# Kernel tuning notes

Measured on AMD Instinct MI355X. Metric: run time of the kernel, lower is better.

## Reference

```python
import jax, jax.numpy as jnp
import numpy as np

RADIUS = 0.2
NSAMPLE = 32
EPS = 1e-5  # BatchNorm2d default eps


def _bn_relu(x, g, b):
    # BatchNorm2d in training mode: per-channel stats over (B, S, nsample), biased var.
    m = x.mean(axis=(0, 1, 2))
    v = jnp.mean((x - m) ** 2, axis=(0, 1, 2))
    return jax.nn.relu((x - m) * jax.lax.rsqrt(v + EPS) * g + b)


def setup_inputs() -> dict:
    key = jax.random.key(0)
    ks = jax.random.split(key, 8)
    B, N, S = 8, 8192, 2048
    xyz = jax.random.uniform(ks[0], (B, 3, N), dtype=jnp.float32)          # unit cube
    points = jax.random.normal(ks[1], (B, 3, N), dtype=jnp.float32)
    fps_idx = jax.random.randint(ks[2], (B, S), 0, N, dtype=jnp.int32)
    W1 = jax.random.normal(ks[3], (64, 6), dtype=jnp.float32) * 0.1
    W2 = jax.random.normal(ks[4], (64, 64), dtype=jnp.float32) * 0.1
    W3 = jax.random.normal(ks[5], (128, 64), dtype=jnp.float32) * 0.1
    return dict(
        xyz=xyz, points=points, fps_idx=fps_idx,
        W1=W1, g1=jnp.ones((64,)), b1=jnp.zeros((64,)),
        W2=W2, g2=jnp.ones((64,)), b2=jnp.zeros((64,)),
        W3=W3, g3=jnp.ones((128,)), b3=jnp.zeros((128,)),
    )


def reference(xyz, points, fps_idx, W1, g1, b1, W2, g2, b2, W3, g3, b3):
    B, _, N = xyz.shape
    xyz_t = jnp.transpose(xyz, (0, 2, 1))            # [B,N,3]
    pts_t = jnp.transpose(points, (0, 2, 1))         # [B,N,D]
    # gather_operation: sampled centers
    new_xyz_t = jnp.take_along_axis(xyz_t, fps_idx[:, :, None], axis=1)  # [B,S,3]
    # ball query: first NSAMPLE points within radius; pad with first hit
    d2 = jnp.sum((new_xyz_t[:, :, None, :] - xyz_t[:, None, :, :]) ** 2, axis=-1)  # [B,S,N]
    keys = jnp.where(d2 <= RADIUS * RADIUS, jnp.arange(N, dtype=jnp.int32), N)
    neg_top, _ = jax.lax.top_k(-keys, NSAMPLE)       # smallest keys first
    idx = -neg_top                                   # [B,S,NSAMPLE]
    idx = jnp.where(idx < N, idx, idx[:, :, 0:1])    # pad empty slots with first hit (self always in-radius)
    bidx = jnp.arange(B)[:, None, None]
    grouped_xyz = xyz_t[bidx, idx]                   # [B,S,ns,3]
    rel = grouped_xyz - new_xyz_t[:, :, None, :]     # center-relative coords
    grouped_pts = pts_t[bidx, idx]                   # [B,S,ns,D]
    feat = jnp.concatenate([rel, grouped_pts], axis=-1)  # [B,S,ns,3+D]
    for W, g, b in ((W1, g1, b1), (W2, g2, b2), (W3, g3, b3)):
        feat = _bn_relu(jnp.einsum('bsnc,oc->bsno', feat, W), g, b)
    new_points = jnp.max(feat, axis=2)               # max over neighbors -> [B,S,C]
    return jnp.transpose(new_xyz_t, (0, 2, 1)), jnp.transpose(new_points, (0, 2, 1))
```

## Files before the change

kernel.cpp:

```cpp
#include <hip/hip_runtime.h>
#include <hip/hip_bf16.h>

#define BB_ 8
#define NN_ 8192
#define SS_ 2048
#define NS 32
#define C1 64
#define C2 64
#define C3 128
#define RAD2 0.04f
#define BN_EPS 1e-5f
#define M_TOT (BB_*SS_*NS)
#define INV_M (1.0f/524288.0f)
#define YSTR 34

typedef __attribute__((ext_vector_type(8))) short bf16x8;
typedef __attribute__((ext_vector_type(4))) float f32x4;

#define FBF_OFF 0
#define WPK_OFF 2097152
#define ST_OFF  2104320
#define GMM_OFF 2104832

__device__ inline unsigned pkbf(float a, float b) {
    __hip_bfloat162 h = __float22bfloat162_rn(make_float2(a, b));
    unsigned r; __builtin_memcpy(&r, &h, 4); return r;
}
__device__ inline bf16x8 asfrag(uint4 v) { bf16x8 r; __builtin_memcpy(&r, &v, 16); return r; }
__device__ inline float bflo(unsigned u) { unsigned x = u << 16; float f; __builtin_memcpy(&f, &x, 4); return f; }
__device__ inline float bfhi(unsigned u) { unsigned x = u & 0xffff0000u; float f; __builtin_memcpy(&f, &x, 4); return f; }

__device__ inline void fin1_ch(const float* __restrict__ st, const float* __restrict__ W1,
                               const float* __restrict__ g, const float* __restrict__ bb,
                               int o, float* __restrict__ al, float* __restrict__ cl) {
    float w[6];
    #pragma unroll
    for (int i = 0; i < 6; ++i) w[i] = W1[o * 6 + i];
    float ms = 0.f;
    #pragma unroll
    for (int i = 0; i < 6; ++i) ms = fmaf(w[i], st[i], ms);
    float m = ms * INV_M;
    float e2 = 0.f;
    #pragma unroll
    for (int ci = 0; ci < 6; ++ci)
        #pragma unroll
        for (int d = 0; d < 6; ++d) {
            int lo = ci < d ? ci : d, hi = ci < d ? d : ci;
            int idx = 6 + lo * 6 - lo * (lo + 1) / 2 + hi;
            e2 = fmaf(w[ci] * w[d], st[idx], e2);
        }
    float var = e2 * INV_M - m * m;
    float ai = g[o] * (1.0f / sqrtf(var + BN_EPS));
    al[o] = ai;
    cl[o] = bb[o] - m * ai;
}

__device__ inline void fin_ch(const float* __restrict__ sum, const float* __restrict__ sq,
                              const float* __restrict__ g, const float* __restrict__ bb,
                              int o, float* __restrict__ al, float* __restrict__ cl) {
    float m = sum[o] * INV_M;
    float var = sq[o] * INV_M - m * m;
    float ai = g[o] * (1.0f / sqrtf(var + BN_EPS));
    al[o] = ai;
    cl[o] = bb[o] - m * ai;
}

__global__ void k_front(const float* __restrict__ xyz, const float* __restrict__ pts,
                        const int* __restrict__ fps, uint4* __restrict__ fbf,
                        const float* __restrict__ W1, const float* __restrict__ W2,
                        const float* __restrict__ W3, uint4* __restrict__ wf,
                        float* __restrict__ st) {
    __shared__ int lidx[4][NS];
    int tid = threadIdx.x;
    if (blockIdx.x >= 4096) {
        int bb = blockIdx.x - 4096;
        if (bb == 7) { st[tid] = 0.f; st[tid + 256] = 0.f; return; }
        int t = bb * 256 + tid;
        int l = t & 63, p = l & 15, qd = l >> 4;
        float v[8];
        if (t < 256) {
            int mt = t >> 6;
            #pragma unroll
            for (int j = 0; j < 8; ++j)
                v[j] = (qd == 0 && j < 6) ? W1[(mt * 16 + p) * 6 + j] : 0.f;
        } else if (t < 768) {
            int fr = (t - 256) >> 6;
            int mt = fr >> 1, kf = fr & 1;
            #pragma unroll
            for (int j = 0; j < 8; ++j)
                v[j] = W2[(16 * mt + p) * 64 + kf * 32 + qd * 8 + j];
        } else {
            int fr = (t - 768) >> 6;
            int nt = fr >> 1, kf = fr & 1;
            #pragma unroll
            for (int j = 0; j < 8; ++j)
                v[j] = W3[(nt * 16 + p) * 64 + kf * 32 + qd * 8 + j];
        }
        uint4 o;
        o.x = pkbf(v[0], v[1]); o.y = pkbf(v[2], v[3]);
        o.z = pkbf(v[4], v[5]); o.w = pkbf(v[6], v[7]);
        wf[t] = o;
        return;
    }
    int wave = (blockIdx.x * blockDim.x + tid) >> 6;
    int lane = tid & 63;
    int wslot = tid >> 6;
    int b = wave / SS_;
    const float* xb = xyz + (size_t)b * 3 * NN_;
    const float* pb = pts + (size_t)b * 3 * NN_;
    int ci = fps[wave];
    float cx = xb[ci], cy = xb[NN_ + ci], cz = xb[2 * NN_ + ci];

    float sx[4], sy[4], sz[4];
    #pragma unroll
    for (int k = 0; k < 4; ++k) {
        sx[k] = xb[k * 64 + lane];
        sy[k] = xb[NN_ + k * 64 + lane];
        sz[k] = xb[2 * NN_ + k * 64 + lane];
    }
    int found = 0;
    int first_i = -1;
    #pragma unroll 1
    for (int base = 0; base < NN_; base += 256) {
        #pragma unroll
        for (int k = 0; k < 4; ++k) {
            float xv = sx[k], yv = sy[k], zv = sz[k];
            int nb = base + 256 + k * 64;
            if (nb >= NN_) nb = 0;
            sx[k] = xb[nb + lane];
            sy[k] = xb[NN_ + nb + lane];
            sz[k] = xb[2 * NN_ + nb + lane];
            float dx = xv - cx, dy = yv - cy, dz = zv - cz;
            float d2 = __fadd_rn(__fadd_rn(__fmul_rn(dx, dx), __fmul_rn(dy, dy)), __fmul_rn(dz, dz));
            bool inr = d2 <= RAD2;
            unsigned long long mask = __ballot(inr);
            if (first_i < 0 && mask) first_i = base + k * 64 + __builtin_ctzll(mask);
            if (inr) {
                int pos = found + __popcll(mask & ((1ull << lane) - 1ull));
                if (pos < NS) lidx[wslot][pos] = base + k * 64 + lane;
            }
            found += __popcll(mask);
        }
        if (found >= NS) break;
    }
    if (found > NS) found = NS;
    if (lane < NS) {
        int j = (lane < found) ? lidx[wslot][lane] : first_i;
        uint4 o;
        o.x = pkbf(xb[j] - cx,           xb[NN_ + j] - cy);
        o.y = pkbf(xb[2 * NN_ + j] - cz, pb[j]);
        o.z = pkbf(pb[NN_ + j],          pb[2 * NN_ + j]);
        o.w = 0u;
        fbf[(size_t)wave * NS + lane] = o;
    }
}

__global__ void k_p1(const uint4* __restrict__ fbf, float* __restrict__ st) {
    __shared__ float sacc[27];
    int tid = threadIdx.x;
    if (tid < 27) sacc[tid] = 0.f;
    __syncthreads();
    int gt = blockIdx.x * 256 + tid;
    float vals[27];
    #pragma unroll
    for (int i = 0; i < 27; ++i) vals[i] = 0.f;
    #pragma unroll 1
    for (int it = 0; it < M_TOT / 262144; ++it) {
        uint4 w = fbf[it * 262144 + gt];
        float f[6] = { bflo(w.x), bfhi(w.x), bflo(w.y), bfhi(w.y), bflo(w.z), bfhi(w.z) };
        #pragma unroll
        for (int c = 0; c < 6; ++c) vals[c] += f[c];
        int q = 6;
        #pragma unroll
        for (int c = 0; c < 6; ++c)
            #pragma unroll
            for (int d = c; d < 6; ++d) { vals[q] = fmaf(f[c], f[d], vals[q]); ++q; }
    }
    int lane = tid & 63;
    #pragma unroll
    for (int i = 0; i < 27; ++i) {
        float v = vals[i];
        #pragma unroll
        for (int d = 32; d; d >>= 1) v += __shfl_xor(v, d);
        if (lane == 0) atomicAdd(&sacc[i], v);
    }
    __syncthreads();
    if (tid < 27) atomicAdd(&st[tid], sacc[tid]);
}

__global__ __launch_bounds__(256, 4) void k_p2(
        const uint4* __restrict__ fbf, const uint4* __restrict__ wpk,
        float* __restrict__ st,
        const float* __restrict__ W1, const float* __restrict__ g1, const float* __restrict__ b1) {
    __shared__ unsigned yls[4][64 * YSTR];
    __shared__ float bs[C2], bq[C2];
    __shared__ float a1ls[C1], c1ls[C1];
    int tid = threadIdx.x, wslot = tid >> 6, lane = tid & 63;
    int p = lane & 15, qd = lane >> 4;
    int tile0 = blockIdx.x * 8 + wslot;
    uint4 bv[4];
    #pragma unroll
    for (int nt = 0; nt < 4; ++nt) {
        uint4 v = make_uint4(0u, 0u, 0u, 0u);
        if (qd == 0) v = fbf[tile0 * 64 + nt * 16 + p];
        bv[nt] = v;
    }
    bf16x8 w1r[4];
    #pragma unroll
    for (int mt = 0; mt < 4; ++mt) w1r[mt] = asfrag(wpk[mt * 64 + lane]);
    if (tid < C2) { bs[tid] = 0.f; bq[tid] = 0.f; fin1_ch(st, W1, g1, b1, tid, a1ls, c1ls); }
    __syncthreads();
    const uint4* w2f = wpk + 256;
    unsigned* my = yls[wslot];
    float s2[4][4], q2[4][4];
    #pragma unroll
    for (int i = 0; i < 4; ++i)
        #pragma unroll
        for (int r = 0; r < 4; ++r) { s2[i][r] = 0.f; q2[i][r] = 0.f; }

    #pragma unroll
    for (int t = 0; t < 2; ++t) {
        uint4 nbv[4];
        if (t == 0) {
            #pragma unroll
            for (int nt = 0; nt < 4; ++nt) {
                uint4 v = make_uint4(0u, 0u, 0u, 0u);
                if (qd == 0) v = fbf[(tile0 + 4) * 64 + nt * 16 + p];
                nbv[nt] = v;
            }
        }
        bf16x8 B1[4];
        #pragma unroll
        for (int nt = 0; nt < 4; ++nt) B1[nt] = asfrag(bv[nt]);
        #pragma unroll
        for (int mt = 0; mt < 4; ++mt) {
            bf16x8 A = w1r[mt];
            float4 av = *(const float4*)(a1ls + mt * 16 + qd * 4);
            float4 cv = *(const float4*)(c1ls + mt * 16 + qd * 4);
            #pragma unroll
            for (int nt = 0; nt < 4; ++nt) {
                f32x4 acc = {0.f, 0.f, 0.f, 0.f};
                acc = __builtin_amdgcn_mfma_f32_16x16x32_bf16(A, B1[nt], acc, 0, 0, 0);
                float y0 = fmaxf(fmaf(av.x, acc[0], cv.x), 0.f);
                float y1 = fmaxf(fmaf(av.y, acc[1], cv.y), 0.f);
                float y2 = fmaxf(fmaf(av.z, acc[2], cv.z), 0.f);
                float y3 = fmaxf(fmaf(av.w, acc[3], cv.w), 0.f);
                int a = (nt * 16 + p) * YSTR + mt * 8 + qd * 2;
                *(uint2*)&my[a] = make_uint2(pkbf(y0, y1), pkbf(y2, y3));
            }
        }
        asm volatile("" ::: "memory");
        bf16x8 B2[4][2];
        #pragma unroll
        for (int nt = 0; nt < 4; ++nt)
            #pragma unroll
            for (int kf = 0; kf < 2; ++kf)
                B2[nt][kf] = asfrag(*(const uint4*)&my[(nt * 16 + p) * YSTR + kf * 16 + qd * 4]);
        asm volatile("" ::: "memory");
        #pragma unroll
        for (int mt = 0; mt < 4; ++mt) {
            f32x4 acc[4];
            #pragma unroll
            for (int nt = 0; nt < 4; ++nt) acc[nt] = (f32x4){0.f, 0.f, 0.f, 0.f};
            #pragma unroll
            for (int kf = 0; kf < 2; ++kf) {
                bf16x8 W = asfrag(w2f[(mt * 2 + kf) * 64 + lane]);
                #pragma unroll
                for (int nt = 0; nt < 4; ++nt)
                    acc[nt] = __builtin_amdgcn_mfma_f32_16x16x32_bf16(W, B2[nt][kf], acc[nt], 0, 0, 0);
            }
            #pragma unroll
            for (int r = 0; r < 4; ++r) {
                float u0 = acc[0][r], u1 = acc[1][r], u2 = acc[2][r], u3 = acc[3][r];
                s2[mt][r] += (u0 + u1) + (u2 + u3);
                q2[mt][r] = fmaf(u0, u0, fmaf(u1, u1, fmaf(u2, u2, fmaf(u3, u3, q2[mt][r]))));
            }
        }
        if (t == 0) {
            #pragma unroll
            for (int nt = 0; nt < 4; ++nt) bv[nt] = nbv[nt];
        }
        asm volatile("" ::: "memory");
    }
    #pragma unroll
    for (int mt = 0; mt < 4; ++mt)
        #pragma unroll
        for (int r = 0; r < 4; ++r) {
            float s = s2[mt][r], q = q2[mt][r];
            #pragma unroll
            for (int off = 1; off <= 8; off <<= 1) { s += __shfl_xor(s, off); q += __shfl_xor(q, off); }
            if (p == 0) {
                atomicAdd(&bs[mt * 16 + qd * 4 + r], s);
                atomicAdd(&bq[mt * 16 + qd * 4 + r], q);
            }
        }
    __syncthreads();
    if (tid < C2) { atomicAdd(&st[64 + tid], bs[tid]); atomicAdd(&st[128 + tid], bq[tid]); }
}

__global__ __launch_bounds__(256, 4) void k_p3_fused(
        const uint4* __restrict__ fbf, const uint4* __restrict__ wpk,
        float* __restrict__ st,
        const float* __restrict__ W1, const float* __restrict__ g1, const float* __restrict__ b1,
        const float* __restrict__ g2, const float* __restrict__ b2,
        const float* __restrict__ g3, float* __restrict__ gmm) {
    __shared__ unsigned yls[4][64 * YSTR];
    __shared__ float bs[C3], bq[C3];
    __shared__ float a1ls[C1], c1ls[C1], a2ls[C2], c2ls[C2];
    int tid = threadIdx.x, wslot = tid >> 6, lane = tid & 63;
    int p = lane & 15, qd = lane >> 4;
    int tile0 = blockIdx.x * 4 + wslot;
    uint4 bv0[4], bv1[4];
    #pragma unroll
    for (int nt = 0; nt < 4; ++nt) {
        uint4 v0 = make_uint4(0u, 0u, 0u, 0u);
        uint4 v1 = make_uint4(0u, 0u, 0u, 0u);
        if (qd == 0) {
            v0 = fbf[tile0 * 64 + nt * 16 + p];
            v1 = fbf[(tile0 + 4096) * 64 + nt * 16 + p];
        }
        bv0[nt] = v0; bv1[nt] = v1;
    }
    unsigned posm = 0;
    #pragma unroll
    for (int i = 0; i < 8; ++i) posm |= (g3[i * 16 + p] >= 0.f) ? (1u << i) : 0u;
    if (tid < 128) bs[tid] = 0.f; else bq[tid - 128] = 0.f;
    if (tid < 64) fin1_ch(st, W1, g1, b1, tid, a1ls, c1ls);
    else if (tid < 128) fin_ch(st + 64, st + 128, g2, b2, tid - 64, a2ls, c2ls);
    __syncthreads();
    const uint4* w1f = wpk;
    const uint4* w2f = wpk + 256;
    const uint4* w3f = wpk + 768;
    unsigned* my = yls[wslot];

    #pragma unroll
    for (int it = 0; it < 2; ++it) {
        int tile = tile0 + it * 4096;
        #pragma unroll
        for (int mt = 0; mt < 4; ++mt) {
            bf16x8 Aw = asfrag(w1f[mt * 64 + lane]);
            float4 av = *(const float4*)(a1ls + mt * 16 + qd * 4);
            float4 cv = *(const float4*)(c1ls + mt * 16 + qd * 4);
            #pragma unroll
            for (int nt = 0; nt < 4; ++nt) {
                uint4 bcur = (it == 0) ? bv0[nt] : bv1[nt];
                f32x4 acc = {0.f, 0.f, 0.f, 0.f};
                acc = __builtin_amdgcn_mfma_f32_16x16x32_bf16(Aw, asfrag(bcur), acc, 0, 0, 0);
                float y0 = fmaxf(fmaf(av.x, acc[0], cv.x), 0.f);
                float y1 = fmaxf(fmaf(av.y, acc[1], cv.y), 0.f);
                float y2 = fmaxf(fmaf(av.z, acc[2], cv.z), 0.f);
                float y3 = fmaxf(fmaf(av.w, acc[3], cv.w), 0.f);
                int a = (nt * 16 + p) * YSTR + mt * 8 + qd * 2;
                *(uint2*)&my[a] = make_uint2(pkbf(y0, y1), pkbf(y2, y3));
            }
        }
        asm volatile("" ::: "memory");
        bf16x8 B2[4][2];
        #pragma unroll
        for (int nt = 0; nt < 4; ++nt)
            #pragma unroll
            for (int kf = 0; kf < 2; ++kf)
                B2[nt][kf] = asfrag(*(const uint4*)&my[(nt * 16 + p) * YSTR + kf * 16 + qd * 4]);
        asm volatile("" ::: "memory");
        #pragma unroll
        for (int mt = 0; mt < 4; ++mt) {
            f32x4 acc[4];
            #pragma unroll
            for (int nt = 0; nt < 4; ++nt) acc[nt] = (f32x4){0.f, 0.f, 0.f, 0.f};
            #pragma unroll
            for (int kf = 0; kf < 2; ++kf) {
                bf16x8 W = asfrag(w2f[(mt * 2 + kf) * 64 + lane]);
                #pragma unroll
                for (int nt = 0; nt < 4; ++nt)
                    acc[nt] = __builtin_amdgcn_mfma_f32_16x16x32_bf16(W, B2[nt][kf], acc[nt], 0, 0, 0);
            }
            float4 av = *(const float4*)(a2ls + mt * 16 + qd * 4);
            float4 cv = *(const float4*)(c2ls + mt * 16 + qd * 4);
            #pragma unroll
            for (int nt = 0; nt < 4; ++nt) {
                float y0 = fmaxf(fmaf(av.x, acc[nt][0], cv.x), 0.f);
                float y1 = fmaxf(fmaf(av.y, acc[nt][1], cv.y), 0.f);
                float y2 = fmaxf(fmaf(av.z, acc[nt][2], cv.z), 0.f);
                float y3 = fmaxf(fmaf(av.w, acc[nt][3], cv.w), 0.f);
                int a = (nt * 16 + p) * YSTR + mt * 8 + qd * 2;
                *(uint2*)&my[a] = make_uint2(pkbf(y0, y1), pkbf(y2, y3));
            }
        }
        asm volatile("" ::: "memory");
        bf16x8 A3[4][2];
        #pragma unroll
        for (int mt = 0; mt < 4; ++mt) {
            A3[mt][0] = asfrag(*(const uint4*)&my[(mt * 16 + p) * YSTR + qd * 4]);
            A3[mt][1] = asfrag(*(const uint4*)&my[(mt * 16 + p) * YSTR + 16 + qd * 4]);
        }
        asm volatile("" ::: "memory");
        uint4 wva = w3f[lane];
        uint4 wvb = w3f[64 + lane];
        #pragma unroll 1
        for (int nt = 0; nt < 8; ++nt) {
            int nn = (nt < 7) ? nt + 1 : 7;
            uint4 nwa = w3f[(nn * 2 + 0) * 64 + lane];
            uint4 nwb = w3f[(nn * 2 + 1) * 64 + lane];
            bf16x8 Wa = asfrag(wva), Wb = asfrag(wvb);
            f32x4 acc[4];
            #pragma unroll
            for (int mt = 0; mt < 4; ++mt) {
                acc[mt] = __builtin_amdgcn_mfma_f32_16x16x32_bf16(A3[mt][0], Wa,
                            (f32x4){0.f, 0.f, 0.f, 0.f}, 0, 0, 0);
                acc[mt] = __builtin_amdgcn_mfma_f32_16x16x32_bf16(A3[mt][1], Wb, acc[mt], 0, 0, 0);
            }
            bool pn = (posm >> nt) & 1;
            float s = 0.f, q = 0.f, va = 0.f, vb = 0.f;
            #pragma unroll
            for (int mt = 0; mt < 4; ++mt) {
                float v0 = acc[mt][0], v1 = acc[mt][1], v2 = acc[mt][2], v3 = acc[mt][3];
                s += (v0 + v1) + (v2 + v3);
                q = fmaf(v0, v0, fmaf(v1, v1, fmaf(v2, v2, fmaf(v3, v3, q))));
                float mx = fmaxf(fmaxf(v0, v1), fmaxf(v2, v3));
                float mn = fminf(fminf(v0, v1), fminf(v2, v3));
                float vv = pn ? mx : -mn;
                if (mt == 0) va = vv;
                else if (mt == 1) va = fmaxf(va, vv);
                else if (mt == 2) vb = vv;
                else vb = fmaxf(vb, vv);
            }
            s += __shfl_xor(s, 16); s += __shfl_xor(s, 32);
            q += __shfl_xor(q, 16); q += __shfl_xor(q, 32);
            va = fmaxf(va, __shfl_xor(va, 16)); va = fmaxf(va, __shfl_xor(va, 32));
            vb = fmaxf(vb, __shfl_xor(vb, 16)); vb = fmaxf(vb, __shfl_xor(vb, 32));
            if (lane < 16) {
                gmm[(size_t)(tile * 2 + 0) * C3 + nt * 16 + lane] = va;
                gmm[(size_t)(tile * 2 + 1) * C3 + nt * 16 + lane] = vb;
                atomicAdd(&bs[nt * 16 + lane], s);
                atomicAdd(&bq[nt * 16 + lane], q);
            }
            wva = nwa; wvb = nwb;
        }
    }
    __syncthreads();
    if (tid < C3) { atomicAdd(&st[192 + tid], bs[tid]); atomicAdd(&st[320 + tid], bq[tid]); }
}

__global__ void k_outx(const float* __restrict__ gmm, const float* __restrict__ st,
                       const float* __restrict__ g3, const float* __restrict__ b3,
                       const float* __restrict__ xyz, const int* __restrict__ fps,
                       float* __restrict__ out) {
    __shared__ float T[C3][17];
    __shared__ float a3ls[C3], c3ls[C3];
    int blk = blockIdx.x, tid = threadIdx.x;
    if (blk < 1024) {
        if (tid < C3) fin_ch(st + 192, st + 320, g3, b3, tid, a3ls, c3ls);
        __syncthreads();
        int b = blk >> 7, s0 = (blk & 127) << 4;
        #pragma unroll
        for (int i = 0; i < 8; ++i) {
            int idx = i * 256 + tid;
            int sl = idx >> 7, o = idx & 127;
            float m = gmm[((size_t)(b * SS_ + s0 + sl)) * C3 + o];
            float a = a3ls[o];
            float v = (a >= 0.f) ? m : -m;
            T[o][sl] = fmaxf(fmaf(a, v, c3ls[o]), 0.f);
        }
        __syncthreads();
        int o = tid & 127, sh = tid >> 7;
        float* dst = out + (size_t)BB_ * 3 * SS_ + ((size_t)b * C3 + o) * SS_ + s0 + sh * 8;
        float4 w0, w1;
        w0.x = T[o][sh * 8 + 0]; w0.y = T[o][sh * 8 + 1];
        w0.z = T[o][sh * 8 + 2]; w0.w = T[o][sh * 8 + 3];
        w1.x = T[o][sh * 8 + 4]; w1.y = T[o][sh * 8 + 5];
        w1.z = T[o][sh * 8 + 6]; w1.w = T[o][sh * 8 + 7];
        *(float4*)dst = w0; *(float4*)(dst + 4) = w1;
    } else {
        int t = (blk - 1024) * 256 + tid;
        int b = t / (3 * SS_);
        int r = (t / SS_) % 3;
        int s = t % SS_;
        int ci = fps[b * SS_ + s];
        out[t] = xyz[((size_t)b * 3 + r) * NN_ + ci];
    }
}

extern "C" void kernel_launch(void* const* d_in, const int* in_sizes, int n_in,
                              void* d_out, int out_size, void* d_ws, size_t ws_size,
                              hipStream_t stream) {
    (void)in_sizes; (void)n_in; (void)out_size; (void)ws_size;
    const float* xyz = (const float*)d_in[0];
    const float* pts = (const float*)d_in[1];
    const int*   fps = (const int*)d_in[2];
    const float* W1 = (const float*)d_in[3];
    const float* g1 = (const float*)d_in[4];
    const float* b1 = (const float*)d_in[5];
    const float* W2 = (const float*)d_in[6];
    const float* g2 = (const float*)d_in[7];
    const float* b2 = (const float*)d_in[8];
    const float* W3 = (const float*)d_in[9];
    const float* g3 = (const float*)d_in[10];
    const float* b3 = (const float*)d_in[11];
    float* out = (float*)d_out;
    float* ws = (float*)d_ws;

    uint4* fbf = (uint4*)(ws + FBF_OFF);
    uint4* wpk = (uint4*)(ws + WPK_OFF);
    float* st  = ws + ST_OFF;
    float* gmm = ws + GMM_OFF;

    k_front<<<4096 + 8, 256, 0, stream>>>(xyz, pts, fps, fbf, W1, W2, W3, wpk, st);
    k_p1<<<1024, 256, 0, stream>>>(fbf, st);
    k_p2<<<1024, 256, 0, stream>>>(fbf, wpk, st, W1, g1, b1);
    k_p3_fused<<<1024, 256, 0, stream>>>(fbf, wpk, st, W1, g1, b1, g2, b2, g3, gmm);
    k_outx<<<1024 + 192, 256, 0, stream>>>(gmm, st, g3, b3, xyz, fps, out);
}
```

Baseline: 233.7 us.

## Halve per-wave work in MLP passes to raise occupancy and block count

```diff
diff --git a/kernel.cpp b/kernel.cpp
--- a/kernel.cpp
+++ b/kernel.cpp
@@ -188,28 +188,26 @@
     if (tid < 27) atomicAdd(&st[tid], sacc[tid]);
 }
 
-__global__ __launch_bounds__(256, 4) void k_p2(
+__global__ __launch_bounds__(256, 8) void k_p2(
         const uint4* __restrict__ fbf, const uint4* __restrict__ wpk,
         float* __restrict__ st,
         const float* __restrict__ W1, const float* __restrict__ g1, const float* __restrict__ b1) {
-    __shared__ unsigned yls[4][64 * YSTR];
+    __shared__ unsigned yls[4][32 * YSTR];
     __shared__ float bs[C2], bq[C2];
     __shared__ float a1ls[C1], c1ls[C1];
     int tid = threadIdx.x, wslot = tid >> 6, lane = tid & 63;
     int p = lane & 15, qd = lane >> 4;
-    int tile0 = blockIdx.x * 8 + wslot;
+    int tile = blockIdx.x * 4 + wslot;
     uint4 bv[4];
     #pragma unroll
     for (int nt = 0; nt < 4; ++nt) {
         uint4 v = make_uint4(0u, 0u, 0u, 0u);
-        if (qd == 0) v = fbf[tile0 * 64 + nt * 16 + p];
+        if (qd == 0) v = fbf[tile * 64 + nt * 16 + p];
         bv[nt] = v;
     }
-    bf16x8 w1r[4];
-    #pragma unroll
-    for (int mt = 0; mt < 4; ++mt) w1r[mt] = asfrag(wpk[mt * 64 + lane]);
     if (tid < C2) { bs[tid] = 0.f; bq[tid] = 0.f; fin1_ch(st, W1, g1, b1, tid, a1ls, c1ls); }
     __syncthreads();
+    const uint4* w1f = wpk;
     const uint4* w2f = wpk + 256;
     unsigned* my = yls[wslot];
     float s2[4][4], q2[4][4];
@@ -219,66 +217,50 @@
         for (int r = 0; r < 4; ++r) { s2[i][r] = 0.f; q2[i][r] = 0.f; }
 
     #pragma unroll
-    for (int t = 0; t < 2; ++t) {
-        uint4 nbv[4];
-        if (t == 0) {
-            #pragma unroll
-            for (int nt = 0; nt < 4; ++nt) {
-                uint4 v = make_uint4(0u, 0u, 0u, 0u);
-                if (qd == 0) v = fbf[(tile0 + 4) * 64 + nt * 16 + p];
-                nbv[nt] = v;
-            }
-        }
-        bf16x8 B1[4];
-        #pragma unroll
-        for (int nt = 0; nt < 4; ++nt) B1[nt] = asfrag(bv[nt]);
+    for (int h = 0; h < 2; ++h) {
         #pragma unroll
         for (int mt = 0; mt < 4; ++mt) {
-            bf16x8 A = w1r[mt];
+            bf16x8 A = asfrag(w1f[mt * 64 + lane]);
             float4 av = *(const float4*)(a1ls + mt * 16 + qd * 4);
             float4 cv = *(const float4*)(c1ls + mt * 16 + qd * 4);
             #pragma unroll
-            for (int nt = 0; nt < 4; ++nt) {
+            for (int ntl = 0; ntl < 2; ++ntl) {
                 f32x4 acc = {0.f, 0.f, 0.f, 0.f};
-                acc = __builtin_amdgcn_mfma_f32_16x16x32_bf16(A, B1[nt], acc, 0, 0, 0);
+                acc = __builtin_amdgcn_mfma_f32_16x16x32_bf16(A, asfrag(bv[h * 2 + ntl]), acc, 0, 0, 0);
                 float y0 = fmaxf(fmaf(av.x, acc[0], cv.x), 0.f);
                 float y1 = fmaxf(fmaf(av.y, acc[1], cv.y), 0.f);
                 float y2 = fmaxf(fmaf(av.z, acc[2], cv.z), 0.f);
                 float y3 = fmaxf(fmaf(av.w, acc[3], cv.w), 0.f);
-                int a = (nt * 16 + p) * YSTR + mt * 8 + qd * 2;
+                int a = (ntl * 16 + p) * YSTR + mt * 8 + qd * 2;
                 *(uint2*)&my[a] = make_uint2(pkbf(y0, y1), pkbf(y2, y3));
             }
         }
         asm volatile("" ::: "memory");
-        bf16x8 B2[4][2];
-        #pragma unroll
-        for (int nt = 0; nt < 4; ++nt)
+        bf16x8 B2[2][2];
+        #pragma unroll
+        for (int ntl = 0; ntl < 2; ++ntl)
             #pragma unroll
             for (int kf = 0; kf < 2; ++kf)
-                B2[nt][kf] = asfrag(*(const uint4*)&my[(nt * 16 + p) * YSTR + kf * 16 + qd * 4]);
+                B2[ntl][kf] = asfrag(*(const uint4*)&my[(ntl * 16 + p) * YSTR + kf * 16 + qd * 4]);
         asm volatile("" ::: "memory");
         #pragma unroll
         for (int mt = 0; mt < 4; ++mt) {
-            f32x4 acc[4];
-            #pragma unroll
-            for (int nt = 0; nt < 4; ++nt) acc[nt] = (f32x4){0.f, 0.f, 0.f, 0.f};
+            f32x4 acc[2];
+            #pragma unroll
+            for (int ntl = 0; ntl < 2; ++ntl) acc[ntl] = (f32x4){0.f, 0.f, 0.f, 0.f};
             #pragma unroll
             for (int kf = 0; kf < 2; ++kf) {
                 bf16x8 W = asfrag(w2f[(mt * 2 + kf) * 64 + lane]);
                 #pragma unroll
-                for (int nt = 0; nt < 4; ++nt)
-                    acc[nt] = __builtin_amdgcn_mfma_f32_16x16x32_bf16(W, B2[nt][kf], acc[nt], 0, 0, 0);
+                for (int ntl = 0; ntl < 2; ++ntl)
+                    acc[ntl] = __builtin_amdgcn_mfma_f32_16x16x32_bf16(W, B2[ntl][kf], acc[ntl], 0, 0, 0);
             }
             #pragma unroll
             for (int r = 0; r < 4; ++r) {
-                float u0 = acc[0][r], u1 = acc[1][r], u2 = acc[2][r], u3 = acc[3][r];
-                s2[mt][r] += (u0 + u1) + (u2 + u3);
-                q2[mt][r] = fmaf(u0, u0, fmaf(u1, u1, fmaf(u2, u2, fmaf(u3, u3, q2[mt][r]))));
-            }
-        }
-        if (t == 0) {
-            #pragma unroll
-            for (int nt = 0; nt < 4; ++nt) bv[nt] = nbv[nt];
+                float u0 = acc[0][r], u1 = acc[1][r];
+                s2[mt][r] += u0 + u1;
+                q2[mt][r] = fmaf(u0, u0, fmaf(u1, u1, q2[mt][r]));
+            }
         }
         asm volatile("" ::: "memory");
     }
@@ -298,28 +280,24 @@
     if (tid < C2) { atomicAdd(&st[64 + tid], bs[tid]); atomicAdd(&st[128 + tid], bq[tid]); }
 }
 
-__global__ __launch_bounds__(256, 4) void k_p3_fused(
+__global__ __launch_bounds__(256, 8) void k_p3_fused(
         const uint4* __restrict__ fbf, const uint4* __restrict__ wpk,
         float* __restrict__ st,
         const float* __restrict__ W1, const float* __restrict__ g1, const float* __restrict__ b1,
         const float* __restrict__ g2, const float* __restrict__ b2,
         const float* __restrict__ g3, float* __restrict__ gmm) {
-    __shared__ unsigned yls[4][64 * YSTR];
+    __shared__ unsigned yls[4][32 * YSTR];
     __shared__ float bs[C3], bq[C3];
     __shared__ float a1ls[C1], c1ls[C1], a2ls[C2], c2ls[C2];
     int tid = threadIdx.x, wslot = tid >> 6, lane = tid & 63;
     int p = lane & 15, qd = lane >> 4;
-    int tile0 = blockIdx.x * 4 + wslot;
-    uint4 bv0[4], bv1[4];
+    int tile = blockIdx.x * 4 + wslot;
+    uint4 bv[4];
     #pragma unroll
     for (int nt = 0; nt < 4; ++nt) {
-        uint4 v0 = make_uint4(0u, 0u, 0u, 0u);
-        uint4 v1 = make_uint4(0u, 0u, 0u, 0u);
-        if (qd == 0) {
-            v0 = fbf[tile0 * 64 + nt * 16 + p];
-            v1 = fbf[(tile0 + 4096) * 64 + nt * 16 + p];
-        }
-        bv0[nt] = v0; bv1[nt] = v1;
+        uint4 v = make_uint4(0u, 0u, 0u, 0u);
+        if (qd == 0) v = fbf[tile * 64 + nt * 16 + p];
+        bv[nt] = v;
     }
     unsigned posm = 0;
     #pragma unroll
@@ -334,64 +312,62 @@
     unsigned* my = yls[wslot];
 
     #pragma unroll
-    for (int it = 0; it < 2; ++it) {
-        int tile = tile0 + it * 4096;
+    for (int h = 0; h < 2; ++h) {
         #pragma unroll
         for (int mt = 0; mt < 4; ++mt) {
             bf16x8 Aw = asfrag(w1f[mt * 64 + lane]);
             float4 av = *(const float4*)(a1ls + mt * 16 + qd * 4);
             float4 cv = *(const float4*)(c1ls + mt * 16 + qd * 4);
             #pragma unroll
-            for (int nt = 0; nt < 4; ++nt) {
-                uint4 bcur = (it == 0) ? bv0[nt] : bv1[nt];
+            for (int ntl = 0; ntl < 2; ++ntl) {
                 f32x4 acc = {0.f, 0.f, 0.f, 0.f};
-                acc = __builtin_amdgcn_mfma_f32_16x16x32_bf16(Aw, asfrag(bcur), acc, 0, 0, 0);
+                acc = __builtin_amdgcn_mfma_f32_16x16x32_bf16(Aw, asfrag(bv[h * 2 + ntl]), acc, 0, 0, 0);
                 float y0 = fmaxf(fmaf(av.x, acc[0], cv.x), 0.f);
                 float y1 = fmaxf(fmaf(av.y, acc[1], cv.y), 0.f);
                 float y2 = fmaxf(fmaf(av.z, acc[2], cv.z), 0.f);
                 float y3 = fmaxf(fmaf(av.w, acc[3], cv.w), 0.f);
-                int a = (nt * 16 + p) * YSTR + mt * 8 + qd * 2;
+                int a = (ntl * 16 + p) * YSTR + mt * 8 + qd * 2;
                 *(uint2*)&my[a] = make_uint2(pkbf(y0, y1), pkbf(y2, y3));
             }
         }
         asm volatile("" ::: "memory");
-        bf16x8 B2[4][2];
-        #pragma unroll
-        for (int nt = 0; nt < 4; ++nt)
+        bf16x8 B2[2][2];
+        #pragma unroll
+        for (int ntl = 0; ntl < 2; ++ntl)
             #pragma unroll
             for (int kf = 0; kf < 2; ++kf)
-                B2[nt][kf] = asfrag(*(const uint4*)&my[(nt * 16 + p) * YSTR + kf * 16 + qd * 4]);
+                B2[ntl][kf] = asfrag(*(const uint4*)&my[(ntl * 16 + p) * YSTR + kf * 16 + qd * 4]);
         asm volatile("" ::: "memory");
         #pragma unroll
         for (int mt = 0; mt < 4; ++mt) {
-            f32x4 acc[4];
-            #pragma unroll
-            for (int nt = 0; nt < 4; ++nt) acc[nt] = (f32x4){0.f, 0.f, 0.f, 0.f};
+            f32x4 acc[2];
+            #pragma unroll
+            for (int ntl = 0; ntl < 2; ++ntl) acc[ntl] = (f32x4){0.f, 0.f, 0.f, 0.f};
             #pragma unroll
             for (int kf = 0; kf < 2; ++kf) {
                 bf16x8 W = asfrag(w2f[(mt * 2 + kf) * 64 + lane]);
                 #pragma unroll
-                for (int nt = 0; nt < 4; ++nt)
-                    acc[nt] = __builtin_amdgcn_mfma_f32_16x16x32_bf16(W, B2[nt][kf], acc[nt], 0, 0, 0);
+                for (int ntl = 0; ntl < 2; ++ntl)
+                    acc[ntl] = __builtin_amdgcn_mfma_f32_16x16x32_bf16(W, B2[ntl][kf], acc[ntl], 0, 0, 0);
             }
             float4 av = *(const float4*)(a2ls + mt * 16 + qd * 4);
             float4 cv = *(const float4*)(c2ls + mt * 16 + qd * 4);
             #pragma unroll
-            for (int nt = 0; nt < 4; ++nt) {
-                float y0 = fmaxf(fmaf(av.x, acc[nt][0], cv.x), 0.f);
-                float y1 = fmaxf(fmaf(av.y, acc[nt][1], cv.y), 0.f);
-                float y2 = fmaxf(fmaf(av.z, acc[nt][2], cv.z), 0.f);
-                float y3 = fmaxf(fmaf(av.w, acc[nt][3], cv.w), 0.f);
-                int a = (nt * 16 + p) * YSTR + mt * 8 + qd * 2;
+            for (int ntl = 0; ntl < 2; ++ntl) {
+                float y0 = fmaxf(fmaf(av.x, acc[ntl][0], cv.x), 0.f);
+                float y1 = fmaxf(fmaf(av.y, acc[ntl][1], cv.y), 0.f);
+                float y2 = fmaxf(fmaf(av.z, acc[ntl][2], cv.z), 0.f);
+                float y3 = fmaxf(fmaf(av.w, acc[ntl][3], cv.w), 0.f);
+                int a = (ntl * 16 + p) * YSTR + mt * 8 + qd * 2;
                 *(uint2*)&my[a] = make_uint2(pkbf(y0, y1), pkbf(y2, y3));
             }
         }
         asm volatile("" ::: "memory");
-        bf16x8 A3[4][2];
-        #pragma unroll
-        for (int mt = 0; mt < 4; ++mt) {
-            A3[mt][0] = asfrag(*(const uint4*)&my[(mt * 16 + p) * YSTR + qd * 4]);
-            A3[mt][1] = asfrag(*(const uint4*)&my[(mt * 16 + p) * YSTR + 16 + qd * 4]);
+        bf16x8 A3[2][2];
+        #pragma unroll
+        for (int mtl = 0; mtl < 2; ++mtl) {
+            A3[mtl][0] = asfrag(*(const uint4*)&my[(mtl * 16 + p) * YSTR + qd * 4]);
+            A3[mtl][1] = asfrag(*(const uint4*)&my[(mtl * 16 + p) * YSTR + 16 + qd * 4]);
         }
         asm volatile("" ::: "memory");
         uint4 wva = w3f[lane];
@@ -402,40 +378,32 @@
             uint4 nwa = w3f[(nn * 2 + 0) * 64 + lane];
             uint4 nwb = w3f[(nn * 2 + 1) * 64 + lane];
             bf16x8 Wa = asfrag(wva), Wb = asfrag(wvb);
-            f32x4 acc[4];
-            #pragma unroll
-            for (int mt = 0; mt < 4; ++mt) {
-                acc[mt] = __builtin_amdgcn_mfma_f32_16x16x32_bf16(A3[mt][0], Wa,
+            bool pn = (posm >> nt) & 1;
+            float s = 0.f, q = 0.f, va = 0.f;
+            #pragma unroll
+            for (int mtl = 0; mtl < 2; ++mtl) {
+                f32x4 acc = __builtin_amdgcn_mfma_f32_16x16x32_bf16(A3[mtl][0], Wa,
                             (f32x4){0.f, 0.f, 0.f, 0.f}, 0, 0, 0);
-                acc[mt] = __builtin_amdgcn_mfma_f32_16x16x32_bf16(A3[mt][1], Wb, acc[mt], 0, 0, 0);
-            }
-            bool pn = (posm >> nt) & 1;
-            float s = 0.f, q = 0.f, va = 0.f, vb = 0.f;
-            #pragma unroll
-            for (int mt = 0; mt < 4; ++mt) {
-                float v0 = acc[mt][0], v1 = acc[mt][1], v2 = acc[mt][2], v3 = acc[mt][3];
+                acc = __builtin_amdgcn_mfma_f32_16x16x32_bf16(A3[mtl][1], Wb, acc, 0, 0, 0);
+                float v0 = acc[0], v1 = acc[1], v2 = acc[2], v3 = acc[3];
                 s += (v0 + v1) + (v2 + v3);
                 q = fmaf(v0, v0, fmaf(v1, v1, fmaf(v2, v2, fmaf(v3, v3, q))));
                 float mx = fmaxf(fmaxf(v0, v1), fmaxf(v2, v3));
                 float mn = fminf(fminf(v0, v1), fminf(v2, v3));
                 float vv = pn ? mx : -mn;
-                if (mt == 0) va = vv;
-                else if (mt == 1) va = fmaxf(va, vv);
-                else if (mt == 2) vb = vv;
-                else vb = fmaxf(vb, vv);
+                va = (mtl == 0) ? vv : fmaxf(va, vv);
             }
             s += __shfl_xor(s, 16); s += __shfl_xor(s, 32);
             q += __shfl_xor(q, 16); q += __shfl_xor(q, 32);
             va = fmaxf(va, __shfl_xor(va, 16)); va = fmaxf(va, __shfl_xor(va, 32));
-            vb = fmaxf(vb, __shfl_xor(vb, 16)); vb = fmaxf(vb, __shfl_xor(vb, 32));
             if (lane < 16) {
-                gmm[(size_t)(tile * 2 + 0) * C3 + nt * 16 + lane] = va;
-                gmm[(size_t)(tile * 2 + 1) * C3 + nt * 16 + lane] = vb;
+                gmm[(size_t)(tile * 2 + h) * C3 + nt * 16 + lane] = va;
                 atomicAdd(&bs[nt * 16 + lane], s);
                 atomicAdd(&bq[nt * 16 + lane], q);
             }
             wva = nwa; wvb = nwb;
         }
+        asm volatile("" ::: "memory");
     }
     __syncthreads();
     if (tid < C3) { atomicAdd(&st[192 + tid], bs[tid]); atomicAdd(&st[320 + tid], bq[tid]); }
@@ -506,7 +474,7 @@
 
     k_front<<<4096 + 8, 256, 0, stream>>>(xyz, pts, fps, fbf, W1, W2, W3, wpk, st);
     k_p1<<<1024, 256, 0, stream>>>(fbf, st);
-    k_p2<<<1024, 256, 0, stream>>>(fbf, wpk, st, W1, g1, b1);
-    k_p3_fused<<<1024, 256, 0, stream>>>(fbf, wpk, st, W1, g1, b1, g2, b2, g3, gmm);
+    k_p2<<<2048, 256, 0, stream>>>(fbf, wpk, st, W1, g1, b1);
+    k_p3_fused<<<2048, 256, 0, stream>>>(fbf, wpk, st, W1, g1, b1, g2, b2, g3, gmm);
     k_outx<<<1024 + 192, 256, 0, stream>>>(gmm, st, g3, b3, xyz, fps, out);
 }
```

Result: slower. 287.2 us (+22.9%).
